# Performance work log

Hardware: AMD Instinct MI355X
Metric: run time of the kernel (lower is better)

Reference implementation:

```python
import jax, jax.numpy as jnp
import numpy as np


def setup_inputs() -> dict:
    key = jax.random.key(0)
    ks = jax.random.split(key, 8)
    B, Tq, S, H = 32, 4, 2048, 1024
    return {
        "query": jax.random.normal(ks[0], (B, Tq, H), dtype=jnp.float32),
        "keys": jax.random.normal(ks[1], (S, B, 2 * H), dtype=jnp.float32),
        "Wa_w": jax.random.normal(ks[2], (H, H), dtype=jnp.float32) * 0.02,
        "Wa_b": jax.random.normal(ks[3], (H,), dtype=jnp.float32) * 0.02,
        "Ua_w": jax.random.normal(ks[4], (H, 2 * H), dtype=jnp.float32) * 0.02,
        "Ua_b": jax.random.normal(ks[5], (H,), dtype=jnp.float32) * 0.02,
        "Va_w": jax.random.normal(ks[6], (1, H), dtype=jnp.float32) * 0.02,
        "Va_b": jax.random.normal(ks[7], (1,), dtype=jnp.float32) * 0.02,
    }


def reference(query, keys, Wa_w, Wa_b, Ua_w, Ua_b, Va_w, Va_b):
    # query: [B, Tq, H] -> last step [B, 1, H]
    q = query[:, -1:, :]
    # keys: [S, B, 2H] -> [B, S, 2H]
    k = jnp.transpose(keys, (1, 0, 2))
    # Additive attention scores: Va(tanh(Wa(q) + Ua(k)))
    wq = q @ Wa_w.T + Wa_b                      # [B, 1, H]
    uk = k @ Ua_w.T + Ua_b                      # [B, S, H]
    scores = jnp.tanh(wq + uk) @ Va_w.T + Va_b  # [B, S, 1]
    scores = jnp.transpose(scores, (0, 2, 1))   # [B, 1, S]
    weights = jax.nn.softmax(scores, axis=-1)   # [B, 1, S]
    context = jnp.einsum('bqs,bsd->bqd', weights, k)  # [B, 1, 2H]
    return (context, weights)
```

## Files before the change

kernel.cpp:

```cpp
#include <hip/hip_runtime.h>
#include <hip/hip_bf16.h>

typedef __attribute__((ext_vector_type(4))) float f32x4;
typedef __attribute__((ext_vector_type(8))) short short8;

#define B_   32
#define S_   2048
#define H_   1024
#define D2_  2048
#define BM   256
#define BN   256
#define BK   32
#define NKT  64
#define TILE_SH 8192


__device__ __forceinline__ short f2bf(float f) {
  unsigned u = __float_as_uint(f);
  u = (u + 0x7fffu + ((u >> 16) & 1u)) >> 16;
  return (short)u;
}

__device__ __forceinline__ float bf2f(short s) {
  return __uint_as_float(((unsigned)(unsigned short)s) << 16);
}

__device__ __forceinline__ short8 cvt8(f32x4 a, f32x4 b) {
  short8 o;
  o[0] = f2bf(a.x); o[1] = f2bf(a.y); o[2] = f2bf(a.z); o[3] = f2bf(a.w);
  o[4] = f2bf(b.x); o[5] = f2bf(b.y); o[6] = f2bf(b.z); o[7] = f2bf(b.w);
  return o;
}

__device__ __forceinline__ float fast_tanh(float x) {
  float e = __builtin_amdgcn_exp2f(x * 2.885390081777927f);
  return 1.0f - 2.0f * __builtin_amdgcn_rcpf(e + 1.0f);
}

__device__ __forceinline__ void gload16(const short* g, short* l) {
  __builtin_amdgcn_global_load_lds((const __attribute__((address_space(1))) void*)g,
                                   (__attribute__((address_space(3))) void*)l, 16, 0, 0);
}

__global__ void k_convert_ua(const float* __restrict__ src, short* __restrict__ dst) {
  int idx = blockIdx.x * 256 + threadIdx.x;
  int unit = idx & 1023;
  int kts  = (idx >> 10) & 63;
  int nt   = idx >> 16;
  int row  = unit >> 2;
  int sl   = unit & 3;
  int q    = sl ^ (row & 3);
  const float* s = src + (size_t)(nt * 256 + row) * D2_ + kts * 32 + q * 8;
  f32x4 a = *(const f32x4*)s;
  f32x4 b = *(const f32x4*)(s + 4);
  *(short8*)(dst + (size_t)idx * 8) = cvt8(a, b);
}

__global__ void k_convert_keys(const float* __restrict__ src, short* __restrict__ dst) {
  int idx = blockIdx.x * 256 + threadIdx.x;
  int unit = idx & 1023;
  int kts  = (idx >> 10) & 63;
  int mt   = idx >> 16;
  int row  = unit >> 2;
  int sl   = unit & 3;
  int q    = sl ^ (row & 3);
  const float* s = src + (size_t)(mt * 256 + row) * D2_ + kts * 32 + q * 8;
  f32x4 a = *(const f32x4*)s;
  f32x4 b = *(const f32x4*)(s + 4);
  *(short8*)(dst + (size_t)idx * 8) = cvt8(a, b);
}

__global__ void k_wq(const float* __restrict__ query, const float* __restrict__ Wa_w,
                     const float* __restrict__ Wa_b, const float* __restrict__ Ua_b,
                     float* __restrict__ wqb) {
  int b = blockIdx.x;
  int hc = blockIdx.y;
  int t = threadIdx.x;
  __shared__ float q[H_];
  for (int i = t; i < H_; i += 256) q[i] = query[(size_t)b * (4 * H_) + 3 * H_ + i];
  __syncthreads();
  int h = hc * 128 + (t >> 1);
  int kh = (t & 1) * 512;
  const float* wr = Wa_w + (size_t)h * H_ + kh;
  float acc = 0.f;
  #pragma unroll 8
  for (int k = 0; k < 512; k += 4) {
    f32x4 wv = *(const f32x4*)(wr + k);
    acc += wv.x * q[kh + k] + wv.y * q[kh + k + 1] + wv.z * q[kh + k + 2] + wv.w * q[kh + k + 3];
  }
  acc += __shfl_xor(acc, 1);
  if ((t & 1) == 0) wqb[b * H_ + h] = acc + Wa_b[h] + Ua_b[h];
}

#define MCL16(mb, AF)                                                                             \
  __builtin_amdgcn_s_setprio(1);                                                                  \
  _Pragma("unroll")                                                                               \
  for (int n = 0; n < 4; ++n) {                                                                   \
    _Pragma("unroll")                                                                             \
    for (int i = 0; i < 4; ++i)                                                                   \
      acc[(mb) + i][n] =                                                                          \
          __builtin_amdgcn_mfma_f32_16x16x32_bf16(AF[i], bf[n], acc[(mb) + i][n], 0, 0, 0);       \
  }                                                                                               \
  __builtin_amdgcn_s_setprio(0);

__global__ __launch_bounds__(512, 2) void k_gemm_score(
    const short* __restrict__ keys_bf, const short* __restrict__ uab_t,
    const float* __restrict__ wqb, const float* __restrict__ va,
    float* __restrict__ scores_p) {
  __shared__ short As[2][TILE_SH];
  __shared__ short Bs[2][TILE_SH];

  const int bid = blockIdx.x;
  const int g = (bid & 7) * 128 + (bid >> 3);
  const int mt = g >> 2;
  const int nt = g & 3;
  const int r0 = mt * BM;
  const int h0 = nt * BN;

  const int t = threadIdx.x;
  const int lane = t & 63;
  const int w = t >> 6;
  const int wm = w >> 2;
  const int wn = w & 3;

  f32x4 acc[8][4] = {};

  const short* abase = keys_bf + (size_t)mt * (NKT * TILE_SH) + t * 8;
  const short* bbase = uab_t  + (size_t)nt * (NKT * TILE_SH) + t * 8;
  const int wu = w * 512;

  const int lr = lane & 15;
  const int lq = lane >> 4;
  const int slot = lq ^ (lr & 3);
  const int aoff = (wm * 128 + lr) * 32 + slot * 8;
  const int boff = (wn * 64 + lr) * 32 + slot * 8;

  {
    gload16(abase,        &As[0][wu]);
    gload16(abase + 4096, &As[0][4096 + wu]);
    gload16(bbase,        &Bs[0][wu]);
    gload16(bbase + 4096, &Bs[0][4096 + wu]);
    asm volatile("s_waitcnt vmcnt(0)" ::: "memory");
    __builtin_amdgcn_s_barrier();
  }

  short8 bf[4], af0[4], af1[4];

  #pragma unroll 1
  for (int kts = 0; kts < NKT; ++kts) {
    const int cb = kts & 1;
    const bool stage = (kts < NKT - 1);
    const short* Ac = As[cb];
    const short* Bc = Bs[cb];
    short* Anb = &As[cb ^ 1][0];
    short* Bnb = &Bs[cb ^ 1][0];
    const short* anext = abase + (size_t)(kts + 1) * TILE_SH;
    const short* bnext = bbase + (size_t)(kts + 1) * TILE_SH;

    #pragma unroll
    for (int n = 0; n < 4; ++n) bf[n] = *(const short8*)&Bc[boff + n * 512];
    #pragma unroll
    for (int i = 0; i < 4; ++i) af0[i] = *(const short8*)&Ac[aoff + i * 512];
    #pragma unroll
    for (int i = 0; i < 4; ++i) af1[i] = *(const short8*)&Ac[aoff + (4 + i) * 512];
    if (stage) {
      gload16(anext,        Anb + wu);
      gload16(anext + 4096, Anb + 4096 + wu);
      gload16(bnext,        Bnb + wu);
      gload16(bnext + 4096, Bnb + 4096 + wu);
    }
    asm volatile("s_waitcnt lgkmcnt(4)" ::: "memory");
    __builtin_amdgcn_sched_barrier(0);
    MCL16(0, af0)
    asm volatile("s_waitcnt lgkmcnt(0)" ::: "memory");
    __builtin_amdgcn_sched_barrier(0);
    MCL16(4, af1)
    asm volatile("s_waitcnt vmcnt(0)" ::: "memory");
    __builtin_amdgcn_s_barrier();
  }

  const int lgrp = lane >> 4;
  const int lc = lane & 15;
  float vah[4];
  #pragma unroll
  for (int n = 0; n < 4; ++n) vah[n] = va[h0 + wn * 64 + n * 16 + lc];
  #pragma unroll
  for (int m = 0; m < 8; ++m) {
    #pragma unroll
    for (int reg = 0; reg < 4; ++reg) {
      int row = wm * 128 + m * 16 + lgrp * 4 + reg;
      int r = r0 + row;
      int bb = r & (B_ - 1);
      const float* wrow = wqb + bb * H_ + h0 + wn * 64 + lc;
      float s = 0.f;
      #pragma unroll
      for (int n = 0; n < 4; ++n)
        s += vah[n] * fast_tanh(acc[m][n][reg] + wrow[n * 16]);
      s += __shfl_xor(s, 1);
      s += __shfl_xor(s, 2);
      s += __shfl_xor(s, 4);
      s += __shfl_xor(s, 8);
      if (lc == 0) scores_p[(size_t)r * 16 + nt * 4 + wn] = s;
    }
  }
}

__global__ __launch_bounds__(512, 2) void k_gemm_rs(
    const float* __restrict__ keys, const short* __restrict__ uab_t,
    const float* __restrict__ wqb, const float* __restrict__ va,
    float* __restrict__ scores_p) {
  __shared__ short As[2][TILE_SH];
  __shared__ short Bs[2][TILE_SH];
  const int bid = blockIdx.x;
  const int g = (bid & 7) * 128 + (bid >> 3);
  const int mt = g >> 2;
  const int nt = g & 3;
  const int r0 = mt * BM;
  const int h0 = nt * BN;
  const int t = threadIdx.x;
  const int lane = t & 63;
  const int w = t >> 6;
  const int wm = w >> 2;
  const int wn = w & 3;
  f32x4 acc[8][4] = {};
  const int arow = t >> 1;
  const int hh = t & 1;
  const float* abase = keys + (size_t)(r0 + arow) * D2_ + hh * 16;
  int awoff[2];
  #pragma unroll
  for (int j = 0; j < 2; ++j)
    awoff[j] = arow * 32 + (((2 * hh + j) ^ (arow & 3)) << 3);
  const short* bbase = uab_t + (size_t)nt * NKT * TILE_SH + t * 8;
  const int wu = w * 512;
  const int lr = lane & 15;
  const int lq = lane >> 4;
  const int slot = lq ^ (lr & 3);
  const int aoff = (wm * 128 + lr) * 32 + slot * 8;
  const int boff = (wn * 64 + lr) * 32 + slot * 8;
  short8 bf[4], af0[4], af1[4];
  {
    f32x4 v0 = *(const f32x4*)(abase);
    f32x4 v1 = *(const f32x4*)(abase + 4);
    f32x4 v2 = *(const f32x4*)(abase + 8);
    f32x4 v3 = *(const f32x4*)(abase + 12);
    *(short8*)&As[0][awoff[0]] = cvt8(v0, v1);
    *(short8*)&As[0][awoff[1]] = cvt8(v2, v3);
    gload16(bbase,        &Bs[0][wu]);
    gload16(bbase + 4096, &Bs[0][4096 + wu]);
    asm volatile("s_waitcnt vmcnt(0) lgkmcnt(0)" ::: "memory");
    __builtin_amdgcn_s_barrier();
  }
  #pragma unroll 1
  for (int kts = 0; kts < NKT; ++kts) {
    const int cb = kts & 1;
    const bool stage = (kts < NKT - 1);
    const float* anext = abase + (kts + 1) * BK;
    const short* bnext = bbase + (size_t)(kts + 1) * TILE_SH;
    short* Anb = &As[cb ^ 1][0];
    short* Bnb = &Bs[cb ^ 1][0];
    const short* Ac = As[cb];
    const short* Bc = Bs[cb];

    #pragma unroll
    for (int n = 0; n < 4; ++n) bf[n] = *(const short8*)&Bc[boff + n * 512];
    #pragma unroll
    for (int i = 0; i < 4; ++i) af0[i] = *(const short8*)&Ac[aoff + i * 512];
    #pragma unroll
    for (int i = 0; i < 4; ++i) af1[i] = *(const short8*)&Ac[aoff + (4 + i) * 512];
    f32x4 v0, v1, v2, v3;
    if (stage) {
      v0 = *(const f32x4*)(anext);
      v1 = *(const f32x4*)(anext + 4);
      v2 = *(const f32x4*)(anext + 8);
      v3 = *(const f32x4*)(anext + 12);
      gload16(bnext,        Bnb + wu);
      gload16(bnext + 4096, Bnb + 4096 + wu);
    }
    asm volatile("s_waitcnt lgkmcnt(4)" ::: "memory");
    __builtin_amdgcn_sched_barrier(0);
    MCL16(0, af0)
    asm volatile("s_waitcnt lgkmcnt(0)" ::: "memory");
    __builtin_amdgcn_sched_barrier(0);
    MCL16(4, af1)
    __builtin_amdgcn_s_barrier();
    if (stage) {
      *(short8*)&Anb[awoff[0]] = cvt8(v0, v1);
      *(short8*)&Anb[awoff[1]] = cvt8(v2, v3);
    }
    asm volatile("s_waitcnt vmcnt(0) lgkmcnt(0)" ::: "memory");
    __builtin_amdgcn_s_barrier();
  }
  const int lgrp = lane >> 4;
  const int lc = lane & 15;
  float vah[4];
  #pragma unroll
  for (int n = 0; n < 4; ++n) vah[n] = va[h0 + wn * 64 + n * 16 + lc];
  #pragma unroll
  for (int m = 0; m < 8; ++m) {
    #pragma unroll
    for (int reg = 0; reg < 4; ++reg) {
      int row = wm * 128 + m * 16 + lgrp * 4 + reg;
      int r = r0 + row;
      int bb = r & (B_ - 1);
      const float* wrow = wqb + bb * H_ + h0 + wn * 64 + lc;
      float s = 0.f;
      #pragma unroll
      for (int n = 0; n < 4; ++n)
        s += vah[n] * fast_tanh(acc[m][n][reg] + wrow[n * 16]);
      s += __shfl_xor(s, 1);
      s += __shfl_xor(s, 2);
      s += __shfl_xor(s, 4);
      s += __shfl_xor(s, 8);
      if (lc == 0) scores_p[(size_t)r * 16 + nt * 4 + wn] = s;
    }
  }
}

__global__ void k_softmax(const float* __restrict__ scores_p, float* __restrict__ out) {
  int b = blockIdx.x;
  int t = threadIdx.x;
  __shared__ float sc[S_];
  __shared__ float red[4];
  float lmax = -3.4e38f;
  #pragma unroll
  for (int i = 0; i < 8; ++i) {
    int s = t + i * 256;
    const float* p = scores_p + ((size_t)s * B_ + b) * 16;
    f32x4 p0 = *(const f32x4*)p;
    f32x4 p1 = *(const f32x4*)(p + 4);
    f32x4 p2 = *(const f32x4*)(p + 8);
    f32x4 p3 = *(const f32x4*)(p + 12);
    f32x4 ps = p0 + p1 + p2 + p3;
    float v = ps.x + ps.y + ps.z + ps.w;
    sc[s] = v;
    lmax = fmaxf(lmax, v);
  }
  #pragma unroll
  for (int o = 32; o >= 1; o >>= 1) lmax = fmaxf(lmax, __shfl_xor(lmax, o));
  if ((t & 63) == 0) red[t >> 6] = lmax;
  __syncthreads();
  float gmax = fmaxf(fmaxf(red[0], red[1]), fmaxf(red[2], red[3]));
  __syncthreads();
  float lsum = 0.f;
  #pragma unroll
  for (int i = 0; i < 8; ++i) {
    int s = t + i * 256;
    float e = __builtin_amdgcn_exp2f((sc[s] - gmax) * 1.4426950408889634f);
    sc[s] = e;
    lsum += e;
  }
  #pragma unroll
  for (int o = 32; o >= 1; o >>= 1) lsum += __shfl_xor(lsum, o);
  if ((t & 63) == 0) red[t >> 6] = lsum;
  __syncthreads();
  float inv = 1.0f / (red[0] + red[1] + red[2] + red[3]);
  for (int i = 0; i < 8; ++i) {
    int s = t + i * 256;
    out[(size_t)65536 + b * S_ + s] = sc[s] * inv;
  }
}

__global__ __launch_bounds__(256) void k_ctx_partial_bf2(const short* __restrict__ keys_bf,
                                                         const float* __restrict__ wts,
                                                         float* __restrict__ cp) {
  const int ktp = blockIdx.x;
  const int mtc = blockIdx.y;
  const int t = threadIdx.x;
  const int cg = t >> 5;
  const int b = t & 31;
  const int kts = ktp * 2 + (cg >> 2);
  const int slot = (cg & 3) ^ (b & 3);
  const float* wbase = wts + (size_t)b * S_ + mtc * 128;
  f32x4 accA = {}, accB = {};
  #pragma unroll 2
  for (int c = 0; c < 16; ++c) {
    const short* tb = keys_bf + ((size_t)((mtc * 16 + c) * 64 + kts)) * TILE_SH + (slot << 3);
    f32x4 w0 = *(const f32x4*)(wbase + c * 8);
    f32x4 w1 = *(const f32x4*)(wbase + c * 8 + 4);
    float wg[8] = {w0.x, w0.y, w0.z, w0.w, w1.x, w1.y, w1.z, w1.w};
    #pragma unroll
    for (int s8 = 0; s8 < 8; ++s8) {
      short8 v = *(const short8*)(tb + (s8 * 32 + b) * 32);
      float wgt = wg[s8];
      accA.x += wgt * bf2f(v[0]); accA.y += wgt * bf2f(v[1]);
      accA.z += wgt * bf2f(v[2]); accA.w += wgt * bf2f(v[3]);
      accB.x += wgt * bf2f(v[4]); accB.y += wgt * bf2f(v[5]);
      accB.z += wgt * bf2f(v[6]); accB.w += wgt * bf2f(v[7]);
    }
  }
  float* o = cp + ((size_t)mtc * B_ + b) * D2_ + ktp * 64 + cg * 8;
  *(f32x4*)o = accA;
  *(f32x4*)(o + 4) = accB;
}

__global__ void k_ctx_partial(const float* __restrict__ keys, const float* __restrict__ wts,
                              float* __restrict__ cp) {
  int b = blockIdx.x;
  int dc = blockIdx.y;
  int scn = blockIdx.z;
  int t = threadIdx.x;
  __shared__ float wl[256];
  int s0 = scn * 256;
  wl[t] = wts[b * S_ + s0 + t];
  __syncthreads();
  int d = dc * 1024 + t * 4;
  f32x4 acc = {};
  #pragma unroll 4
  for (int i = 0; i < 256; ++i) {
    int s = s0 + i;
    f32x4 kv = *(const f32x4*)(keys + ((size_t)s * B_ + b) * D2_ + d);
    acc += kv * wl[i];
  }
  *(f32x4*)(cp + ((size_t)scn * B_ + b) * D2_ + d) = acc;
}

__global__ void k_ctx_reduce(const float* __restrict__ cp, float* __restrict__ out, int np) {
  int i = blockIdx.x * 256 + threadIdx.x;
  float s = 0.f;
  for (int j = 0; j < np; ++j) s += cp[(size_t)j * 65536 + i];
  out[i] = s;
}

extern "C" void kernel_launch(void* const* d_in, const int* in_sizes, int n_in,
                              void* d_out, int out_size, void* d_ws, size_t ws_size,
                              hipStream_t stream) {
  const float* query = (const float*)d_in[0];
  const float* keys  = (const float*)d_in[1];
  const float* Wa_w  = (const float*)d_in[2];
  const float* Wa_b  = (const float*)d_in[3];
  const float* Ua_w  = (const float*)d_in[4];
  const float* Ua_b  = (const float*)d_in[5];
  const float* Va_w  = (const float*)d_in[6];
  float* out = (float*)d_out;
  char* ws = (char*)d_ws;

  const size_t KEYS_BF_BYTES = 268435456ull;
  const size_t TAIL = 16ull * 1024 * 1024;
  bool big = ws_size >= KEYS_BF_BYTES + TAIL;

  if (big) {
    short* keys_bf = (short*)ws;
    char* base = ws + KEYS_BF_BYTES;
    short* uab_t = (short*)(base);
    float* wqb = (float*)(base + 4u * 1024 * 1024);
    float* sp  = (float*)(base + 4u * 1024 * 1024 + 128 * 1024);
    float* cp  = (float*)(base + 8u * 1024 * 1024 + 256 * 1024);

    hipLaunchKernelGGL(k_convert_ua, dim3(1024), dim3(256), 0, stream, Ua_w, uab_t);
    hipLaunchKernelGGL(k_convert_keys, dim3(65536), dim3(256), 0, stream, keys, keys_bf);
    hipLaunchKernelGGL(k_wq, dim3(32, 8), dim3(256), 0, stream, query, Wa_w, Wa_b, Ua_b, wqb);
    hipLaunchKernelGGL(k_gemm_score, dim3(1024), dim3(512), 0, stream, keys_bf, uab_t, wqb, Va_w, sp);
    hipLaunchKernelGGL(k_softmax, dim3(32), dim3(256), 0, stream, sp, out);
    hipLaunchKernelGGL(k_ctx_partial_bf2, dim3(32, 16), dim3(256), 0, stream, keys_bf, out + 65536, cp);
    hipLaunchKernelGGL(k_ctx_reduce, dim3(256), dim3(256), 0, stream, cp, out, 16);
  } else {
    short* uab_t = (short*)(ws);
    float* wqb = (float*)(ws + 4u * 1024 * 1024);
    float* sp  = (float*)(ws + 4u * 1024 * 1024 + 128 * 1024);
    float* cp  = (float*)(ws + 8u * 1024 * 1024 + 256 * 1024);

    hipLaunchKernelGGL(k_convert_ua, dim3(1024), dim3(256), 0, stream, Ua_w, uab_t);
    hipLaunchKernelGGL(k_wq, dim3(32, 8), dim3(256), 0, stream, query, Wa_w, Wa_b, Ua_b, wqb);
    hipLaunchKernelGGL(k_gemm_rs, dim3(1024), dim3(512), 0, stream, keys, uab_t, wqb, Va_w, sp);
    hipLaunchKernelGGL(k_softmax, dim3(32), dim3(256), 0, stream, sp, out);
    hipLaunchKernelGGL(k_ctx_partial, dim3(32, 2, 8), dim3(256), 0, stream, keys, out + 65536, cp);
    hipLaunchKernelGGL(k_ctx_reduce, dim3(256), dim3(256), 0, stream, cp, out, 8);
  }
}
```

Baseline: 523.0 us.

## Triple-buffer GEMM LDS tiles and change swizzle to row-pair XOR

```diff
diff --git a/kernel.cpp b/kernel.cpp
--- a/kernel.cpp
+++ b/kernel.cpp
@@ -49,7 +49,7 @@
   int nt   = idx >> 16;
   int row  = unit >> 2;
   int sl   = unit & 3;
-  int q    = sl ^ (row & 3);
+  int q    = sl ^ ((row >> 1) & 3);
   const float* s = src + (size_t)(nt * 256 + row) * D2_ + kts * 32 + q * 8;
   f32x4 a = *(const f32x4*)s;
   f32x4 b = *(const f32x4*)(s + 4);
@@ -63,7 +63,7 @@
   int mt   = idx >> 16;
   int row  = unit >> 2;
   int sl   = unit & 3;
-  int q    = sl ^ (row & 3);
+  int q    = sl ^ ((row >> 1) & 3);
   const float* s = src + (size_t)(mt * 256 + row) * D2_ + kts * 32 + q * 8;
   f32x4 a = *(const f32x4*)s;
   f32x4 b = *(const f32x4*)(s + 4);
@@ -107,8 +107,8 @@
     const short* __restrict__ keys_bf, const short* __restrict__ uab_t,
     const float* __restrict__ wqb, const float* __restrict__ va,
     float* __restrict__ scores_p) {
-  __shared__ short As[2][TILE_SH];
-  __shared__ short Bs[2][TILE_SH];
+  __shared__ short As[3][TILE_SH];
+  __shared__ short Bs[3][TILE_SH];
 
   const int bid = blockIdx.x;
   const int g = (bid & 7) * 128 + (bid >> 3);
@@ -131,52 +131,63 @@
 
   const int lr = lane & 15;
   const int lq = lane >> 4;
-  const int slot = lq ^ (lr & 3);
+  const int slot = lq ^ ((lr >> 1) & 3);
   const int aoff = (wm * 128 + lr) * 32 + slot * 8;
   const int boff = (wn * 64 + lr) * 32 + slot * 8;
 
   {
-    gload16(abase,        &As[0][wu]);
-    gload16(abase + 4096, &As[0][4096 + wu]);
-    gload16(bbase,        &Bs[0][wu]);
-    gload16(bbase + 4096, &Bs[0][4096 + wu]);
-    asm volatile("s_waitcnt vmcnt(0)" ::: "memory");
+    gload16(abase,                  &As[0][wu]);
+    gload16(abase + 4096,           &As[0][4096 + wu]);
+    gload16(bbase,                  &Bs[0][wu]);
+    gload16(bbase + 4096,           &Bs[0][4096 + wu]);
+    gload16(abase + TILE_SH,        &As[1][wu]);
+    gload16(abase + TILE_SH + 4096, &As[1][4096 + wu]);
+    gload16(bbase + TILE_SH,        &Bs[1][wu]);
+    gload16(bbase + TILE_SH + 4096, &Bs[1][4096 + wu]);
+    asm volatile("s_waitcnt vmcnt(4)" ::: "memory");
     __builtin_amdgcn_s_barrier();
   }
 
   short8 bf[4], af0[4], af1[4];
+  int cur = 0;
 
   #pragma unroll 1
   for (int kts = 0; kts < NKT; ++kts) {
-    const int cb = kts & 1;
-    const bool stage = (kts < NKT - 1);
-    const short* Ac = As[cb];
-    const short* Bc = Bs[cb];
-    short* Anb = &As[cb ^ 1][0];
-    short* Bnb = &Bs[cb ^ 1][0];
-    const short* anext = abase + (size_t)(kts + 1) * TILE_SH;
-    const short* bnext = bbase + (size_t)(kts + 1) * TILE_SH;
+    int stg = cur + 2; if (stg >= 3) stg -= 3;
+    const short* Ac = &As[cur][0];
+    const short* Bc = &Bs[cur][0];
 
     #pragma unroll
     for (int n = 0; n < 4; ++n) bf[n] = *(const short8*)&Bc[boff + n * 512];
     #pragma unroll
     for (int i = 0; i < 4; ++i) af0[i] = *(const short8*)&Ac[aoff + i * 512];
     #pragma unroll
-    for (int i = 0; i < 4; ++i) af1[i] = *(const short8*)&Ac[aoff + (4 + i) * 512];
-    if (stage) {
-      gload16(anext,        Anb + wu);
-      gload16(anext + 4096, Anb + 4096 + wu);
-      gload16(bnext,        Bnb + wu);
-      gload16(bnext + 4096, Bnb + 4096 + wu);
-    }
+    for (int i = 0; i < 4; ++i) af1[i] = *(const short8*)&Ac[aoff + 2048 + i * 512];
+
+    if (kts < NKT - 2) {
+      const short* an = abase + (size_t)(kts + 2) * TILE_SH;
+      const short* bn = bbase + (size_t)(kts + 2) * TILE_SH;
+      gload16(an,        &As[stg][wu]);
+      gload16(an + 4096, &As[stg][4096 + wu]);
+      gload16(bn,        &Bs[stg][wu]);
+      gload16(bn + 4096, &Bs[stg][4096 + wu]);
+    }
+
     asm volatile("s_waitcnt lgkmcnt(4)" ::: "memory");
     __builtin_amdgcn_sched_barrier(0);
     MCL16(0, af0)
     asm volatile("s_waitcnt lgkmcnt(0)" ::: "memory");
     __builtin_amdgcn_sched_barrier(0);
     MCL16(4, af1)
-    asm volatile("s_waitcnt vmcnt(0)" ::: "memory");
-    __builtin_amdgcn_s_barrier();
+
+    if (kts < NKT - 2) {
+      asm volatile("s_waitcnt vmcnt(4)" ::: "memory");
+    } else if (kts == NKT - 2) {
+      asm volatile("s_waitcnt vmcnt(0)" ::: "memory");
+    }
+    if (kts < NKT - 1) __builtin_amdgcn_s_barrier();
+
+    cur = (cur == 2) ? 0 : cur + 1;
   }
 
   const int lgrp = lane >> 4;
@@ -229,12 +240,12 @@
   int awoff[2];
   #pragma unroll
   for (int j = 0; j < 2; ++j)
-    awoff[j] = arow * 32 + (((2 * hh + j) ^ (arow & 3)) << 3);
+    awoff[j] = arow * 32 + (((2 * hh + j) ^ ((arow >> 1) & 3)) << 3);
   const short* bbase = uab_t + (size_t)nt * NKT * TILE_SH + t * 8;
   const int wu = w * 512;
   const int lr = lane & 15;
   const int lq = lane >> 4;
-  const int slot = lq ^ (lr & 3);
+  const int slot = lq ^ ((lr >> 1) & 3);
   const int aoff = (wm * 128 + lr) * 32 + slot * 8;
   const int boff = (wn * 64 + lr) * 32 + slot * 8;
   short8 bf[4], af0[4], af1[4];
@@ -266,7 +277,7 @@
     #pragma unroll
     for (int i = 0; i < 4; ++i) af0[i] = *(const short8*)&Ac[aoff + i * 512];
     #pragma unroll
-    for (int i = 0; i < 4; ++i) af1[i] = *(const short8*)&Ac[aoff + (4 + i) * 512];
+    for (int i = 0; i < 4; ++i) af1[i] = *(const short8*)&Ac[aoff + 2048 + i * 512];
     f32x4 v0, v1, v2, v3;
     if (stage) {
       v0 = *(const f32x4*)(anext);
@@ -369,7 +380,7 @@
   const int cg = t >> 5;
   const int b = t & 31;
   const int kts = ktp * 2 + (cg >> 2);
-  const int slot = (cg & 3) ^ (b & 3);
+  const int slot = (cg & 3) ^ ((b >> 1) & 3);
   const float* wbase = wts + (size_t)b * S_ + mtc * 128;
   f32x4 accA = {}, accB = {};
   #pragma unroll 2
@@ -388,7 +399,7 @@
       accB.z += wgt * bf2f(v[6]); accB.w += wgt * bf2f(v[7]);
     }
   }
-  float* o = cp + ((size_t)mtc * B_ + b) * D2_ + ktp * 64 + cg * 8;
+  float* o = cp + ((size_t)mtc * B_ + b) * D2_ + ktp * 64 + (cg & 3) * 8 + (cg >> 2) * 32;
   *(f32x4*)o = accA;
   *(f32x4*)(o + 4) = accB;
 }
```

Result: faster. 477.5 us (-8.7%).
